# Kernel optimization log

Hardware: AMD Instinct MI355X
Metric: run time of the kernel (lower is better)

## Reference

```python
import jax, jax.numpy as jnp
import numpy as np
from jax import lax

DIM = 1024
N = 8192

def setup_inputs() -> dict:
    key = jax.random.key(0)
    ks = jax.random.split(key, 7)
    ifeats = jax.random.normal(ks[0], (N, DIM), dtype=jnp.float32)
    tfeat_n = jax.random.normal(ks[1], (1, DIM), dtype=jnp.float32)
    tfeat_a = jax.random.normal(ks[2], (1, DIM), dtype=jnp.float32)
    # Conv2d(1, 2, kernel_size=(3,5), padding=(0,2)) params, OIHW
    fan_in_c = 1 * 3 * 5
    bc = 1.0 / np.sqrt(fan_in_c)
    conv_w = jax.random.uniform(ks[3], (2, 1, 3, 5), minval=-bc, maxval=bc, dtype=jnp.float32)
    conv_b = jax.random.uniform(ks[4], (2,), minval=-bc, maxval=bc, dtype=jnp.float32)
    # Linear(2*dim, dim)
    bl = 1.0 / np.sqrt(2 * DIM)
    w2 = jax.random.uniform(ks[5], (DIM, 2 * DIM), minval=-bl, maxval=bl, dtype=jnp.float32)
    b2 = jax.random.uniform(ks[6], (DIM,), minval=-bl, maxval=bl, dtype=jnp.float32)
    return {"ifeats": ifeats, "tfeat_n": tfeat_n, "tfeat_a": tfeat_a,
            "conv_w": conv_w, "conv_b": conv_b, "w2": w2, "b2": b2}

def reference(ifeats, tfeat_n, tfeat_a, conv_w, conv_b, w2, b2):
    n, d = ifeats.shape
    # Batch the per-sample loop: feats_i = [tfeat_n; tfeat_a; ifeats[i]] -> [N,1,3,D]
    tn = jnp.broadcast_to(tfeat_n, (n, d))
    ta = jnp.broadcast_to(tfeat_a, (n, d))
    x1 = jnp.stack([tn, ta, ifeats], axis=1)[:, None]  # [N,1,3,D]
    # Conv2d(1->2, k=(3,5), pad=(0,2)): height collapses 3->1, width D preserved
    x2 = lax.conv_general_dilated(x1, conv_w, window_strides=(1, 1),
                                  padding=((0, 0), (2, 2)),
                                  dimension_numbers=("NCHW", "OIHW", "NCHW"))
    x2 = x2 + conv_b[None, :, None, None]              # [N,2,1,D]
    x2 = jax.nn.gelu(x2, approximate=False)            # torch nn.GELU() is exact
    x2 = x2.reshape(n, 2 * d)                          # channel-major flatten, matches view(1,-1)
    x3 = x2 @ w2.T + b2                                # Linear(2D -> D)
    return ifeats + x3
```

## Files before the change

### kernel.cpp

```cpp
#include <hip/hip_runtime.h>
#include <cstdint>

#define DIMD 1024
#define NROWS 8192
#define KDIM 2048

typedef unsigned short u16;
typedef __bf16 bf16x8 __attribute__((ext_vector_type(8)));
typedef float f32x4 __attribute__((ext_vector_type(4)));

__device__ __forceinline__ u16 f2bf(float f) {
  unsigned u = __builtin_bit_cast(unsigned, f);
  return (u16)((u + 0x7FFFu + ((u >> 16) & 1u)) >> 16);
}

__device__ __forceinline__ float gelu_exact(float x) {
  float s = 0.70710678118654752f * x;
  float a = fabsf(s);
  float k = __fdividef(1.0f, fmaf(0.3275911f, a, 1.0f));
  float p = 1.061405429f;
  p = fmaf(p, k, -1.453152027f);
  p = fmaf(p, k, 1.421413741f);
  p = fmaf(p, k, -0.284496736f);
  p = fmaf(p, k, 0.254829592f);
  p = p * k;
  float e = __expf(-s * s);
  float erf_s = copysignf(fmaf(-p, e, 1.0f), s);
  return 0.5f * x * (1.0f + erf_s);
}

__global__ __launch_bounds__(256) void pre_kernel(
    const float* __restrict__ ifeats, const float* __restrict__ tn,
    const float* __restrict__ ta, const float* __restrict__ cw,
    const float* __restrict__ cb, const float* __restrict__ w2,
    u16* __restrict__ x2, u16* __restrict__ w2b) {
  const int b = blockIdx.x;
  const int t = threadIdx.x;
  if (b < 1024) {
    const int c = t >> 7;
    const int w0 = (t & 127) << 3;
    float cwn[5], cwa[5], cwi[5];
#pragma unroll
    for (int k = 0; k < 5; ++k) {
      cwn[k] = cw[c * 15 + k];
      cwa[k] = cw[c * 15 + 5 + k];
      cwi[k] = cw[c * 15 + 10 + k];
    }
    const float bias = cb[c];
    float base[8];
    {
      float wn[12], wa[12];
#pragma unroll
      for (int j = 0; j < 12; ++j) {
        int wp = w0 - 2 + j;
        bool ok = (wp >= 0) && (wp < DIMD);
        wn[j] = ok ? tn[ok ? wp : 0] : 0.f;
        wa[j] = ok ? ta[ok ? wp : 0] : 0.f;
      }
#pragma unroll
      for (int s = 0; s < 8; ++s) {
        float x = bias;
#pragma unroll
        for (int k = 0; k < 5; ++k) {
          x = fmaf(cwn[k], wn[s + k], x);
          x = fmaf(cwa[k], wa[s + k], x);
        }
        base[s] = x;
      }
    }
    const bool has_l = (w0 > 0);
    const bool has_r = (w0 < DIMD - 8);
#pragma unroll 1
    for (int r = 0; r < 8; ++r) {
      const int row = b * 8 + r;
      const float* irow = ifeats + (size_t)row * DIMD;
      float wi[12];
      float4 m0 = *(const float4*)(irow + w0);
      float4 m1 = *(const float4*)(irow + w0 + 4);
      wi[0] = has_l ? irow[w0 - 2] : 0.f;
      wi[1] = has_l ? irow[w0 - 1] : 0.f;
      wi[2] = m0.x; wi[3] = m0.y; wi[4] = m0.z; wi[5] = m0.w;
      wi[6] = m1.x; wi[7] = m1.y; wi[8] = m1.z; wi[9] = m1.w;
      wi[10] = has_r ? irow[w0 + 8] : 0.f;
      wi[11] = has_r ? irow[w0 + 9] : 0.f;
      union { u16 o[8]; uint4 u; } pk;
#pragma unroll
      for (int s = 0; s < 8; ++s) {
        float x = base[s];
#pragma unroll
        for (int k = 0; k < 5; ++k) x = fmaf(cwi[k], wi[s + k], x);
        pk.o[s] = f2bf(gelu_exact(x));
      }
      *(uint4*)(x2 + (size_t)row * KDIM + c * DIMD + w0) = pk.u;
    }
  } else {
    const int t2 = (b - 1024) * 256 + t;
    const float4* p = (const float4*)(w2 + (size_t)t2 * 8);
    float4 a = p[0], bb = p[1];
    union { u16 o[8]; uint4 v; } pk;
    pk.o[0] = f2bf(a.x);  pk.o[1] = f2bf(a.y);  pk.o[2] = f2bf(a.z);  pk.o[3] = f2bf(a.w);
    pk.o[4] = f2bf(bb.x); pk.o[5] = f2bf(bb.y); pk.o[6] = f2bf(bb.z); pk.o[7] = f2bf(bb.w);
    *(uint4*)(w2b + (size_t)t2 * 8) = pk.v;
  }
}

__device__ __forceinline__ void gl_lds16(const u16* g, u16* l) {
  __builtin_amdgcn_global_load_lds(
      (__attribute__((address_space(1))) void*)g,
      (__attribute__((address_space(3))) void*)l, 16, 0, 0);
}

#define BK 64
#define BM 256
#define BN 128
#define NTILE 32

#define GITER(T, AVC, BVC, AVN, BVN)                                           \
  {                                                                            \
    if ((T) + 1 < NTILE) {                                                     \
      _Pragma("unroll") for (int mt = 0; mt < 4; ++mt)                         \
        _Pragma("unroll") for (int ks = 0; ks < 2; ++ks)                       \
          AVN[mt][ks] = *(const bf16x8*)&pa1[(wm + mt * 16 + r16) * BK +       \
                                             (((ks * 4 + quad) ^ sw) << 3)];   \
      _Pragma("unroll") for (int nt = 0; nt < 4; ++nt)                         \
        _Pragma("unroll") for (int ks = 0; ks < 2; ++ks)                       \
          BVN[nt][ks] = *(const bf16x8*)&pb1[(wn + nt * 16 + r16) * BK +       \
                                             (((ks * 4 + quad) ^ sw) << 3)];   \
    }                                                                          \
    if ((T) + 3 < NTILE) {                                                     \
      _Pragma("unroll") for (int u = 0; u < 4; ++u)                            \
        gl_lds16(gA[u] + ((T) + 3) * BK, pa0 + (wv * 32 + u * 8) * BK);        \
      _Pragma("unroll") for (int u = 0; u < 2; ++u)                            \
        gl_lds16(gB[u] + ((T) + 3) * BK, pb0 + (wv * 16 + u * 8) * BK);        \
    }                                                                          \
    __builtin_amdgcn_sched_barrier(0);                                         \
    __builtin_amdgcn_s_setprio(1);                                             \
    _Pragma("unroll") for (int ks = 0; ks < 2; ++ks)                           \
      _Pragma("unroll") for (int mt = 0; mt < 4; ++mt)                         \
        _Pragma("unroll") for (int nt = 0; nt < 4; ++nt)                       \
          acc[mt][nt] = __builtin_amdgcn_mfma_f32_16x16x32_bf16(               \
              AVC[mt][ks], BVC[nt][ks], acc[mt][nt], 0, 0, 0);                 \
    __builtin_amdgcn_s_setprio(0);                                             \
    if ((T) + 3 < NTILE) asm volatile("s_waitcnt vmcnt(6)" ::: "memory");      \
    else                 asm volatile("s_waitcnt vmcnt(0)" ::: "memory");      \
    asm volatile("s_waitcnt lgkmcnt(0)" ::: "memory");                         \
    __builtin_amdgcn_s_barrier();                                              \
    __builtin_amdgcn_sched_barrier(0);                                         \
    u16* x_;                                                                   \
    x_ = pa0; pa0 = pa1; pa1 = pa2; pa2 = x_;                                  \
    x_ = pb0; pb0 = pb1; pb1 = pb2; pb2 = x_;                                  \
  }

__global__ __launch_bounds__(512, 1) void gemm_bt(
    const u16* __restrict__ A,
    const u16* __restrict__ B,
    const float* __restrict__ ifeats,
    const float* __restrict__ b2,
    float* __restrict__ out) {
  constexpr int K = KDIM;
  __shared__ __align__(16) u16 sA[3][BM * BK];
  __shared__ __align__(16) u16 sB[3][BN * BK];

  const int tid = threadIdx.x;
  const int wv = tid >> 6;
  const int lane = tid & 63;
  const int id = blockIdx.x;
  const int xcd = id & 7;
  const int s_ = id >> 3;
  const int i0 = (xcd * 4 + (s_ >> 3)) * BM;
  const int j0 = (s_ & 7) * BN;

  const int wm = (wv >> 1) * 64;
  const int wn = (wv & 1) * 64;
  const int quad = lane >> 4;
  const int r16 = lane & 15;
  const int sw = r16 & 7;

  const int srow = lane >> 3;
  const int schunk = (lane & 7) ^ srow;
  const u16* gA[4];
  const u16* gB[2];
#pragma unroll
  for (int u = 0; u < 4; ++u)
    gA[u] = A + (size_t)(i0 + wv * 32 + u * 8 + srow) * K + schunk * 8;
#pragma unroll
  for (int u = 0; u < 2; ++u)
    gB[u] = B + (size_t)(j0 + wv * 16 + u * 8 + srow) * K + schunk * 8;

  const f32x4 vzero = {0.f, 0.f, 0.f, 0.f};
  f32x4 acc[4][4];
#pragma unroll
  for (int a = 0; a < 4; ++a)
#pragma unroll
    for (int b = 0; b < 4; ++b) acc[a][b] = vzero;

  u16* pa0 = (u16*)sA[0]; u16* pa1 = (u16*)sA[1]; u16* pa2 = (u16*)sA[2];
  u16* pb0 = (u16*)sB[0]; u16* pb1 = (u16*)sB[1]; u16* pb2 = (u16*)sB[2];

  bf16x8 avX[4][2], bvX[4][2], avY[4][2], bvY[4][2];

#pragma unroll
  for (int tt = 0; tt < 3; ++tt) {
    u16* ba = (tt == 0) ? pa0 : (tt == 1) ? pa1 : pa2;
    u16* bb = (tt == 0) ? pb0 : (tt == 1) ? pb1 : pb2;
#pragma unroll
    for (int u = 0; u < 4; ++u)
      gl_lds16(gA[u] + tt * BK, ba + (wv * 32 + u * 8) * BK);
#pragma unroll
    for (int u = 0; u < 2; ++u)
      gl_lds16(gB[u] + tt * BK, bb + (wv * 16 + u * 8) * BK);
  }
  asm volatile("s_waitcnt vmcnt(6)" ::: "memory");
  __builtin_amdgcn_s_barrier();
#pragma unroll
  for (int mt = 0; mt < 4; ++mt)
#pragma unroll
    for (int ks = 0; ks < 2; ++ks)
      avX[mt][ks] = *(const bf16x8*)&pa0[(wm + mt * 16 + r16) * BK +
                                         (((ks * 4 + quad) ^ sw) << 3)];
#pragma unroll
  for (int nt = 0; nt < 4; ++nt)
#pragma unroll
    for (int ks = 0; ks < 2; ++ks)
      bvX[nt][ks] = *(const bf16x8*)&pb0[(wn + nt * 16 + r16) * BK +
                                         (((ks * 4 + quad) ^ sw) << 3)];
  asm volatile("s_waitcnt lgkmcnt(0)" ::: "memory");
  __builtin_amdgcn_s_barrier();
  __builtin_amdgcn_sched_barrier(0);

  for (int t = 0; t < NTILE; t += 2) {
    GITER(t,     avX, bvX, avY, bvY);
    GITER(t + 1, avY, bvY, avX, bvX);
  }

#pragma unroll
  for (int nt = 0; nt < 4; ++nt) {
    int col = j0 + wn + nt * 16 + r16;
    float bias = b2[col];
#pragma unroll
    for (int mt = 0; mt < 4; ++mt) {
      int rbase = i0 + wm + mt * 16 + quad * 4;
#pragma unroll
      for (int r = 0; r < 4; ++r) {
        size_t idx = (size_t)(rbase + r) * DIMD + col;
        out[idx] = ifeats[idx] + bias + acc[mt][nt][r];
      }
    }
  }
}

extern "C" void kernel_launch(void* const* d_in, const int* in_sizes, int n_in,
                              void* d_out, int out_size, void* d_ws, size_t ws_size,
                              hipStream_t stream) {
  const float* ifeats = (const float*)d_in[0];
  const float* tn     = (const float*)d_in[1];
  const float* ta     = (const float*)d_in[2];
  const float* cw     = (const float*)d_in[3];
  const float* cb     = (const float*)d_in[4];
  const float* w2     = (const float*)d_in[5];
  const float* b2     = (const float*)d_in[6];
  float* out = (float*)d_out;

  u16* w2b = (u16*)d_ws;
  u16* x2  = (u16*)((char*)d_ws + (size_t)DIMD * KDIM * 2);

  pre_kernel<<<2048, 256, 0, stream>>>(ifeats, tn, ta, cw, cb, w2, x2, w2b);
  gemm_bt<<<256, 512, 0, stream>>>(x2, w2b, ifeats, b2, out);
}
```

Baseline: 153.9 us.

## Prefetch ifeats epilogue tile into LDS during final GEMM iterations

The residual ifeats tile is now staged into shared memory with async global-to-LDS loads, issued during the last three K iterations into LDS buffers that are no longer needed. The epilogue reads it from LDS through an XOR swizzle instead of doing scattered global loads. The aim is to hide the epilogue's global read latency behind the tail MFMAs. In exchange, the vmcnt bookkeeping and buffer-reuse timing become fragile, since ifeats overwrites A buffers that may still be in use.

```diff
diff --git a/kernel.cpp b/kernel.cpp
--- a/kernel.cpp
+++ b/kernel.cpp
@@ -115,9 +115,11 @@
 #define BN 128
 #define NTILE 32
 
-#define GITER(T, AVC, BVC, AVN, BVN)                                           \
+#define VMW(N) asm volatile("s_waitcnt vmcnt(" #N ")" ::: "memory")
+
+#define GITER(T, AVC, BVC, AVN, BVN, FNEXT, STG, VMN, ...)                     \
   {                                                                            \
-    if ((T) + 1 < NTILE) {                                                     \
+    if (FNEXT) {                                                               \
       _Pragma("unroll") for (int mt = 0; mt < 4; ++mt)                         \
         _Pragma("unroll") for (int ks = 0; ks < 2; ++ks)                       \
           AVN[mt][ks] = *(const bf16x8*)&pa1[(wm + mt * 16 + r16) * BK +       \
@@ -127,7 +129,8 @@
           BVN[nt][ks] = *(const bf16x8*)&pb1[(wn + nt * 16 + r16) * BK +       \
                                              (((ks * 4 + quad) ^ sw) << 3)];   \
     }                                                                          \
-    if ((T) + 3 < NTILE) {                                                     \
+    __VA_ARGS__;                                                               \
+    if (STG) {                                                                 \
       _Pragma("unroll") for (int u = 0; u < 4; ++u)                            \
         gl_lds16(gA[u] + ((T) + 3) * BK, pa0 + (wv * 32 + u * 8) * BK);        \
       _Pragma("unroll") for (int u = 0; u < 2; ++u)                            \
@@ -141,8 +144,7 @@
           acc[mt][nt] = __builtin_amdgcn_mfma_f32_16x16x32_bf16(               \
               AVC[mt][ks], BVC[nt][ks], acc[mt][nt], 0, 0, 0);                 \
     __builtin_amdgcn_s_setprio(0);                                             \
-    if ((T) + 3 < NTILE) asm volatile("s_waitcnt vmcnt(6)" ::: "memory");      \
-    else                 asm volatile("s_waitcnt vmcnt(0)" ::: "memory");      \
+    VMW(VMN);                                                                  \
     asm volatile("s_waitcnt lgkmcnt(0)" ::: "memory");                         \
     __builtin_amdgcn_s_barrier();                                              \
     __builtin_amdgcn_sched_barrier(0);                                         \
@@ -158,8 +160,7 @@
     const float* __restrict__ b2,
     float* __restrict__ out) {
   constexpr int K = KDIM;
-  __shared__ __align__(16) u16 sA[3][BM * BK];
-  __shared__ __align__(16) u16 sB[3][BN * BK];
+  __shared__ __align__(16) u16 smem[73728];
 
   const int tid = threadIdx.x;
   const int wv = tid >> 6;
@@ -194,8 +195,15 @@
 #pragma unroll
     for (int b = 0; b < 4; ++b) acc[a][b] = vzero;
 
-  u16* pa0 = (u16*)sA[0]; u16* pa1 = (u16*)sA[1]; u16* pa2 = (u16*)sA[2];
-  u16* pb0 = (u16*)sB[0]; u16* pb1 = (u16*)sB[1]; u16* pb2 = (u16*)sB[2];
+  u16* pa0 = smem;         u16* pa1 = smem + 16384; u16* pa2 = smem + 32768;
+  u16* pb0 = smem + 49152; u16* pb1 = smem + 57344; u16* pb2 = smem + 65536;
+
+  auto if_stage = [&](int r0) {
+    const int row = r0 + wv * 2 + (lane >> 5);
+    const int gch = (lane & 31) ^ (row & 7);
+    gl_lds16((const u16*)(ifeats + (size_t)(i0 + row) * DIMD + j0 + gch * 4),
+             smem + (size_t)(r0 + wv * 2) * 256);
+  };
 
   bf16x8 avX[4][2], bvX[4][2], avY[4][2], bvY[4][2];
 
@@ -228,22 +236,38 @@
   __builtin_amdgcn_s_barrier();
   __builtin_amdgcn_sched_barrier(0);
 
-  for (int t = 0; t < NTILE; t += 2) {
-    GITER(t,     avX, bvX, avY, bvY);
-    GITER(t + 1, avY, bvY, avX, bvX);
-  }
+  for (int t = 0; t < 28; t += 2) {
+    GITER(t,     avX, bvX, avY, bvY, 1, 1, 6, (void)0);
+    GITER(t + 1, avY, bvY, avX, bvX, 1, 1, 6, (void)0);
+  }
+  GITER(28, avX, bvX, avY, bvY, 1, 1, 6, (void)0);
+  GITER(29, avY, bvY, avX, bvX, 1, 0, 4,
+        if_stage(128); if_stage(144); if_stage(160); if_stage(176));
+  GITER(30, avX, bvX, avY, bvY, 1, 0, 10,
+        if_stage(0); if_stage(16); if_stage(32); if_stage(48);
+        if_stage(192); if_stage(208));
+  GITER(31, avY, bvY, avX, bvX, 0, 0, 0,
+        if_stage(64); if_stage(80); if_stage(96); if_stage(112);
+        if_stage(224); if_stage(240));
 
 #pragma unroll
   for (int nt = 0; nt < 4; ++nt) {
     int col = j0 + wn + nt * 16 + r16;
+    int c_in = wn + nt * 16 + r16;
+    int g = c_in >> 2;
     float bias = b2[col];
 #pragma unroll
     for (int mt = 0; mt < 4; ++mt) {
       int rbase = i0 + wm + mt * 16 + quad * 4;
+      int rloc = wm + mt * 16 + quad * 4;
 #pragma unroll
       for (int r = 0; r < 4; ++r) {
+        int row = rloc + r;
+        const float* fp = (const float*)&smem[row * 256 +
+                                              ((g ^ (row & 7)) << 3) +
+                                              ((c_in & 3) << 1)];
         size_t idx = (size_t)(rbase + r) * DIMD + col;
-        out[idx] = ifeats[idx] + bias + acc[mt][nt][r];
+        out[idx] = *fp + bias + acc[mt][nt][r];
       }
     }
   }
```

Measured after the change: 150.6 us. 1.02x faster.
